# Kernel tuning notes

Measured on AMD Instinct MI355X. Metric: run time of the kernel, lower is better.

## Reference

```python
import jax, jax.numpy as jnp
import numpy as np

B, S, D, H = 2, 2048, 1024, 16
DH = D // H  # 64


def setup_inputs() -> dict:
    key = jax.random.key(0)
    ks = jax.random.split(key, 9)
    s = 1.0 / np.sqrt(D)
    return {
        "x": jax.random.normal(ks[0], (B, S, D), dtype=jnp.float32),
        "Wq": jax.random.normal(ks[1], (D, D), dtype=jnp.float32) * s,
        "bq": jnp.zeros((D,), dtype=jnp.float32),
        "Wk": jax.random.normal(ks[2], (D, D), dtype=jnp.float32) * s,
        "bk": jnp.zeros((D,), dtype=jnp.float32),
        "Wv": jax.random.normal(ks[3], (D, D), dtype=jnp.float32) * s,
        "bv": jnp.zeros((D,), dtype=jnp.float32),
        "Wo": jax.random.normal(ks[4], (D, D), dtype=jnp.float32) * s,
        "bo": jnp.zeros((D,), dtype=jnp.float32),
    }


def _split_heads(t):
    # [B, S, D] -> [B, H, S, DH]
    return t.reshape(B, S, H, DH).transpose(0, 2, 1, 3)


def reference(x, Wq, bq, Wk, bk, Wv, bv, Wo, bo):
    q = _split_heads(x @ Wq + bq)
    k = _split_heads(x @ Wk + bk)
    v = _split_heads(x @ Wv + bv)
    scale = 1.0 / jnp.sqrt(jnp.asarray(DH, dtype=x.dtype))
    # [B, H, S, S] score matrix (materialized, as in the original)
    logits = jnp.einsum("bhqd,bhkd->bhqk", q, k) * scale
    attn = jax.nn.softmax(logits, axis=-1)
    out = jnp.einsum("bhqk,bhkd->bhqd", attn, v)
    out = out.transpose(0, 2, 1, 3).reshape(B, S, D)
    return out @ Wo + bo
```

## Files before the change

### kernel.cpp

```cpp
#include <hip/hip_runtime.h>
#include <hip/hip_bf16.h>
#include <stdint.h>


typedef __attribute__((ext_vector_type(8))) short bf16x8;
typedef __attribute__((ext_vector_type(4))) float f32x4;

__device__ __forceinline__ void gld16(const void* g, void* l) {
  __builtin_amdgcn_global_load_lds((const __attribute__((address_space(1))) void*)g,
                                   (__attribute__((address_space(3))) void*)l, 16, 0, 0);
}

__device__ __forceinline__ unsigned short f2b(float f) {
  __hip_bfloat16 h = __float2bfloat16(f);
  return *reinterpret_cast<unsigned short*>(&h);
}

__global__ __launch_bounds__(256) void prep_kernel(const float* __restrict__ x,
                                                   const float* __restrict__ Wq,
                                                   const float* __restrict__ Wk,
                                                   const float* __restrict__ Wv,
                                                   const float* __restrict__ Wo,
                                                   unsigned short* __restrict__ xb,
                                                   unsigned short* __restrict__ wt) {
  __shared__ unsigned short Ls[64 * 72];
  int bid = blockIdx.x;
  int t = threadIdx.x;
  if (bid < 4096) {
    int i = (bid * 256 + t) * 4;
    float4 v = *(const float4*)(x + i);
    ushort4 o = make_ushort4(f2b(v.x), f2b(v.y), f2b(v.z), f2b(v.w));
    *(ushort4*)(xb + i) = o;
    return;
  }
  int tid = bid - 4096;
  int z = tid >> 8, rem = tid & 255;
  int bx = rem & 15, by = rem >> 4;
  const float* src = (z == 0) ? Wq : (z == 1) ? Wk : (z == 2) ? Wv : Wo;
  unsigned short* dst = wt + (size_t)z * 1024 * 1024;
  int k0 = bx * 64, n0 = by * 64;
  int c4 = t & 15;
#pragma unroll
  for (int it = 0; it < 4; ++it) {
    int row = it * 16 + (t >> 4);
    float4 v = *(const float4*)(src + (k0 + row) * 1024 + n0 + c4 * 4);
    Ls[(c4 * 4 + 0) * 72 + row] = f2b(v.x);
    Ls[(c4 * 4 + 1) * 72 + row] = f2b(v.y);
    Ls[(c4 * 4 + 2) * 72 + row] = f2b(v.z);
    Ls[(c4 * 4 + 3) * 72 + row] = f2b(v.w);
  }
  __syncthreads();
  int nr = t >> 2, kc = (t & 3) * 16;
  *(uint4*)(dst + (size_t)(n0 + nr) * 1024 + k0 + kc) = *(uint4*)&Ls[nr * 72 + kc];
  *(uint4*)(dst + (size_t)(n0 + nr) * 1024 + k0 + kc + 8) = *(uint4*)&Ls[nr * 72 + kc + 8];
}

__global__ __launch_bounds__(256) void gemm_qkv(const unsigned short* __restrict__ Ab,
                                                const unsigned short* __restrict__ Bt,
                                                const float* __restrict__ bq,
                                                const float* __restrict__ bk,
                                                const float* __restrict__ bv,
                                                unsigned short* __restrict__ qb,
                                                unsigned short* __restrict__ kb,
                                                unsigned short* __restrict__ vtb) {
  __shared__ unsigned short As[128 * 32];
  __shared__ unsigned short Bs[128 * 32];
  __shared__ unsigned short Es[128 * 72];
  const int t = threadIdx.x;
  const int lane = t & 63, wave = t >> 6;
  const int m0 = blockIdx.x * 128, n0 = blockIdx.y * 128;
  const int wr = (wave >> 1) * 64, wc = (wave & 1) * 64;
  const int fr = lane & 15, fq = lane >> 4;
  f32x4 acc[4][4] = {};
  for (int kt = 0; kt < 32; ++kt) {
    const unsigned short* Ag = Ab + (size_t)m0 * 1024 + kt * 32;
    const unsigned short* Bg = Bt + (size_t)n0 * 1024 + kt * 32;
#pragma unroll
    for (int rep = 0; rep < 2; ++rep) {
      int c = t + rep * 256;
      int row = c >> 2, col = (c & 3) * 8;
      gld16(Ag + (size_t)row * 1024 + col, (void*)(As + c * 8));
      gld16(Bg + (size_t)row * 1024 + col, (void*)(Bs + c * 8));
    }
    __syncthreads();
    bf16x8 a[4], b[4];
#pragma unroll
    for (int i = 0; i < 4; ++i) a[i] = *(const bf16x8*)&As[(wr + i * 16 + fr) * 32 + fq * 8];
#pragma unroll
    for (int j = 0; j < 4; ++j) b[j] = *(const bf16x8*)&Bs[(wc + j * 16 + fr) * 32 + fq * 8];
#pragma unroll
    for (int i = 0; i < 4; ++i)
#pragma unroll
      for (int j = 0; j < 4; ++j)
        acc[i][j] = __builtin_amdgcn_mfma_f32_16x16x32_bf16(a[i], b[j], acc[i][j], 0, 0, 0);
    __syncthreads();
  }
  const int which = n0 >> 10;
  const int bidx = m0 >> 11, s0 = m0 & 2047;
  if (which == 2) {
#pragma unroll
    for (int nh = 0; nh < 2; ++nh) {
      if ((wc >> 6) == nh) {
#pragma unroll
        for (int j = 0; j < 4; ++j) {
          int col = j * 16 + fr;
          float bias = bv[(n0 + nh * 64 + col) & 1023];
#pragma unroll
          for (int i = 0; i < 4; ++i) {
            int sl = wr + i * 16 + fq * 4;
            ushort4 pk;
            pk.x = f2b(acc[i][j][0] + bias);
            pk.y = f2b(acc[i][j][1] + bias);
            pk.z = f2b(acc[i][j][2] + bias);
            pk.w = f2b(acc[i][j][3] + bias);
            *(uint2*)&Es[col * 136 + sl] = *(uint2*)&pk;
          }
        }
      }
      __syncthreads();
      int h = ((n0 + nh * 64) & 1023) >> 6;
#pragma unroll
      for (int it = 0; it < 4; ++it) {
        int dh = it * 16 + (t >> 4);
        int ck = (t & 15) * 8;
        uint4 vv = *(uint4*)&Es[dh * 136 + ck];
        *(uint4*)&vtb[(size_t)((bidx * 16 + h) * 64 + dh) * 2048 + s0 + ck] = vv;
      }
      __syncthreads();
    }
  } else {
    unsigned short* dst = (which == 0) ? qb : kb;
    const float* bias_p = (which == 0) ? bq : bk;
    float scale = (which == 0) ? 0.1803368801111204f : 1.0f;
#pragma unroll
    for (int nh = 0; nh < 2; ++nh) {
      if ((wc >> 6) == nh) {
#pragma unroll
        for (int j = 0; j < 4; ++j) {
          int col = j * 16 + fr;
          float bias = bias_p[(n0 + nh * 64 + col) & 1023];
#pragma unroll
          for (int i = 0; i < 4; ++i)
#pragma unroll
            for (int r = 0; r < 4; ++r) {
              int sl = wr + i * 16 + fq * 4 + r;
              Es[sl * 72 + col] = f2b((acc[i][j][r] + bias) * scale);
            }
        }
      }
      __syncthreads();
      int h = ((n0 + nh * 64) & 1023) >> 6;
#pragma unroll
      for (int it = 0; it < 4; ++it) {
        int sl = it * 32 + (t >> 3);
        int ck = (t & 7) * 8;
        uint4 vv = *(uint4*)&Es[sl * 72 + ck];
        *(uint4*)&dst[(size_t)((bidx * 16 + h) * 2048 + s0 + sl) * 64 + ck] = vv;
      }
      __syncthreads();
    }
  }
}

__global__ __launch_bounds__(256, 2) void attn_kernel(const unsigned short* __restrict__ qb,
                                                      const unsigned short* __restrict__ kb,
                                                      const unsigned short* __restrict__ vtb,
                                                      unsigned short* __restrict__ attn) {
  __shared__ unsigned short Ks[2 * 4096];
  __shared__ unsigned short Vs[2 * 4096];
  __shared__ unsigned short Ps[4 * 2048];
  const int t = threadIdx.x, lane = t & 63, w = t >> 6;
  const int fr = lane & 15, fq = lane >> 4;
  const int bh = blockIdx.y, q0 = blockIdx.x * 128;
  const unsigned short* qg = qb + (size_t)bh * 2048 * 64;
  const unsigned short* kg0 = kb + (size_t)bh * 2048 * 64;
  const unsigned short* vg0 = vtb + (size_t)bh * 64 * 2048;

  bf16x8 qf[2][2];
#pragma unroll
  for (int nb = 0; nb < 2; ++nb)
#pragma unroll
    for (int kk = 0; kk < 2; ++kk)
      qf[nb][kk] = *(const bf16x8*)(qg + (size_t)(q0 + w * 32 + nb * 16 + fr) * 64 + kk * 32 + fq * 8);

  bf16x8 ones;
#pragma unroll
  for (int i = 0; i < 8; ++i) ones[i] = (short)0x3F80;

  f32x4 oacc[2][4] = {};
  f32x4 lacc[2] = {};
  unsigned short* Pw = Ps + w * 2048;

  {
#pragma unroll
    for (int rep = 0; rep < 2; ++rep) {
      int c = t + rep * 256;
      int kk = c >> 8, row = (c >> 2) & 63, cc = c & 3;
      gld16(kg0 + row * 64 + kk * 32 + cc * 8, (void*)(Ks + c * 8));
      gld16(vg0 + (size_t)row * 2048 + kk * 32 + cc * 8, (void*)(Vs + c * 8));
    }
  }

  for (int kt = 0; kt < 32; ++kt) {
    int buf = kt & 1;
    __syncthreads();
    if (kt + 1 < 32) {
      const unsigned short* kg = kg0 + (size_t)(kt + 1) * 4096;
      const unsigned short* vg = vg0 + (kt + 1) * 64;
      int lb = (buf ^ 1) * 4096;
#pragma unroll
      for (int rep = 0; rep < 2; ++rep) {
        int c = t + rep * 256;
        int kk = c >> 8, row = (c >> 2) & 63, cc = c & 3;
        gld16(kg + row * 64 + kk * 32 + cc * 8, (void*)(Ks + lb + c * 8));
        gld16(vg + (size_t)row * 2048 + kk * 32 + cc * 8, (void*)(Vs + lb + c * 8));
      }
    }
    const unsigned short* Kb = Ks + buf * 4096;
    const unsigned short* Vb = Vs + buf * 4096;
    f32x4 sacc[4][2] = {};
#pragma unroll
    for (int kk = 0; kk < 2; ++kk) {
      bf16x8 kf[4];
#pragma unroll
      for (int m = 0; m < 4; ++m) kf[m] = *(const bf16x8*)&Kb[kk * 2048 + (m * 16 + fr) * 32 + fq * 8];
#pragma unroll
      for (int m = 0; m < 4; ++m)
#pragma unroll
        for (int nb = 0; nb < 2; ++nb)
          sacc[m][nb] = __builtin_amdgcn_mfma_f32_16x16x32_bf16(kf[m], qf[nb][kk], sacc[m][nb], 0, 0, 0);
    }
#pragma unroll
    for (int m = 0; m < 4; ++m)
#pragma unroll
      for (int nb = 0; nb < 2; ++nb) {
        int qw = nb * 16 + fr;
        int G = (m * 2 + (fq >> 1)) ^ (qw & 7);
        ushort4 pk;
        pk.x = f2b(__builtin_amdgcn_exp2f(sacc[m][nb][0]));
        pk.y = f2b(__builtin_amdgcn_exp2f(sacc[m][nb][1]));
        pk.z = f2b(__builtin_amdgcn_exp2f(sacc[m][nb][2]));
        pk.w = f2b(__builtin_amdgcn_exp2f(sacc[m][nb][3]));
        *(uint2*)&Pw[qw * 64 + G * 8 + (fq & 1) * 4] = *(uint2*)&pk;
      }
#pragma unroll
    for (int kk = 0; kk < 2; ++kk) {
      bf16x8 pf[2];
#pragma unroll
      for (int mb = 0; mb < 2; ++mb) {
        int qw = mb * 16 + fr;
        int G = (kk * 4 + fq) ^ (qw & 7);
        pf[mb] = *(const bf16x8*)&Pw[qw * 64 + G * 8];
      }
#pragma unroll
      for (int n = 0; n < 4; ++n) {
        bf16x8 vf = *(const bf16x8*)&Vb[kk * 2048 + (n * 16 + fr) * 32 + fq * 8];
#pragma unroll
        for (int mb = 0; mb < 2; ++mb)
          oacc[mb][n] = __builtin_amdgcn_mfma_f32_16x16x32_bf16(pf[mb], vf, oacc[mb][n], 0, 0, 0);
      }
#pragma unroll
      for (int mb = 0; mb < 2; ++mb)
        lacc[mb] = __builtin_amdgcn_mfma_f32_16x16x32_bf16(pf[mb], ones, lacc[mb], 0, 0, 0);
    }
  }
  int bidx = bh >> 4, h = bh & 15;
#pragma unroll
  for (int mb = 0; mb < 2; ++mb)
#pragma unroll
    for (int r = 0; r < 4; ++r) {
      float inv = 1.f / lacc[mb][r];
      int s = q0 + w * 32 + mb * 16 + fq * 4 + r;
      size_t base = (size_t)(bidx * 2048 + s) * 1024 + h * 64;
#pragma unroll
      for (int n = 0; n < 4; ++n) attn[base + n * 16 + fr] = f2b(oacc[mb][n][r] * inv);
    }
}

__global__ __launch_bounds__(256) void gemm_out(const unsigned short* __restrict__ Ab,
                                                const unsigned short* __restrict__ Bt,
                                                const float* __restrict__ bo,
                                                float* __restrict__ out) {
  __shared__ unsigned short As[128 * 32];
  __shared__ unsigned short Bs[128 * 32];
  const int t = threadIdx.x;
  const int lane = t & 63, wave = t >> 6;
  const int m0 = blockIdx.x * 128, n0 = blockIdx.y * 128;
  const int wr = (wave >> 1) * 64, wc = (wave & 1) * 64;
  const int fr = lane & 15, fq = lane >> 4;
  f32x4 acc[4][4] = {};
  for (int kt = 0; kt < 32; ++kt) {
    const unsigned short* Ag = Ab + (size_t)m0 * 1024 + kt * 32;
    const unsigned short* Bg = Bt + (size_t)n0 * 1024 + kt * 32;
#pragma unroll
    for (int rep = 0; rep < 2; ++rep) {
      int c = t + rep * 256;
      int row = c >> 2, col = (c & 3) * 8;
      gld16(Ag + (size_t)row * 1024 + col, (void*)(As + c * 8));
      gld16(Bg + (size_t)row * 1024 + col, (void*)(Bs + c * 8));
    }
    __syncthreads();
    bf16x8 a[4], b[4];
#pragma unroll
    for (int i = 0; i < 4; ++i) a[i] = *(const bf16x8*)&As[(wr + i * 16 + fr) * 32 + fq * 8];
#pragma unroll
    for (int j = 0; j < 4; ++j) b[j] = *(const bf16x8*)&Bs[(wc + j * 16 + fr) * 32 + fq * 8];
#pragma unroll
    for (int i = 0; i < 4; ++i)
#pragma unroll
      for (int j = 0; j < 4; ++j)
        acc[i][j] = __builtin_amdgcn_mfma_f32_16x16x32_bf16(a[i], b[j], acc[i][j], 0, 0, 0);
    __syncthreads();
  }
#pragma unroll
  for (int j = 0; j < 4; ++j) {
    int gn = n0 + wc + j * 16 + fr;
    float bias = bo[gn];
#pragma unroll
    for (int i = 0; i < 4; ++i)
#pragma unroll
      for (int r = 0; r < 4; ++r) {
        int gm = m0 + wr + i * 16 + fq * 4 + r;
        out[(size_t)gm * 1024 + gn] = acc[i][j][r] + bias;
      }
  }
}

extern "C" void kernel_launch(void* const* d_in, const int* in_sizes, int n_in,
                              void* d_out, int out_size, void* d_ws, size_t ws_size,
                              hipStream_t stream) {
  const float* x = (const float*)d_in[0];
  const float* Wq = (const float*)d_in[1];
  const float* bq = (const float*)d_in[2];
  const float* Wk = (const float*)d_in[3];
  const float* bk = (const float*)d_in[4];
  const float* Wv = (const float*)d_in[5];
  const float* bv = (const float*)d_in[6];
  const float* Wo = (const float*)d_in[7];
  const float* bo = (const float*)d_in[8];
  float* out = (float*)d_out;

  unsigned short* ws = (unsigned short*)d_ws;
  const size_t MI = (size_t)1024 * 1024;
  unsigned short* xb = ws;
  unsigned short* wt = ws + 4 * MI;
  unsigned short* qb = wt + 4 * MI;
  unsigned short* kb = qb + 4 * MI;
  unsigned short* vtb = kb + 4 * MI;
  unsigned short* attn = xb;

  prep_kernel<<<5120, 256, 0, stream>>>(x, Wq, Wk, Wv, Wo, xb, wt);
  gemm_qkv<<<dim3(32, 24), 256, 0, stream>>>(xb, wt, bq, bk, bv, qb, kb, vtb);
  attn_kernel<<<dim3(16, 32), 256, 0, stream>>>(qb, kb, vtb, attn);
  gemm_out<<<dim3(32, 8), 256, 0, stream>>>(attn, wt + 3 * MI, bo, out);
}
```

Measured before the change: 209.3 us.

## Split attention keys across waves with 32x32 MFMA and register-resident P

Restructures the attention kernel so each wave handles all 128 queries but a disjoint 32-key slice of each key tile. Scores use 32x32x16 MFMAs, and probabilities stay in registers via a cross-half shuffle instead of round-tripping through LDS. Partial outputs and row sums are reduced across waves through shared memory at the end. Per-wave K/V loads use XOR swizzling and have no double buffering or block barrier in the main loop, so load latency is no longer hidden by prefetch and there is extra reduction work in the epilogue.

```diff
diff --git a/kernel.cpp b/kernel.cpp
--- a/kernel.cpp
+++ b/kernel.cpp
@@ -5,6 +5,7 @@
 
 typedef __attribute__((ext_vector_type(8))) short bf16x8;
 typedef __attribute__((ext_vector_type(4))) float f32x4;
+typedef __attribute__((ext_vector_type(16))) float f32x16;
 
 __device__ __forceinline__ void gld16(const void* g, void* l) {
   __builtin_amdgcn_global_load_lds((const __attribute__((address_space(1))) void*)g,
@@ -14,6 +15,10 @@
 __device__ __forceinline__ unsigned short f2b(float f) {
   __hip_bfloat16 h = __float2bfloat16(f);
   return *reinterpret_cast<unsigned short*>(&h);
+}
+
+__device__ __forceinline__ unsigned int pk2(float a, float b) {
+  return (unsigned int)f2b(a) | ((unsigned int)f2b(b) << 16);
 }
 
 __global__ __launch_bounds__(256) void prep_kernel(const float* __restrict__ x,
@@ -166,115 +171,127 @@
                                                       const unsigned short* __restrict__ kb,
                                                       const unsigned short* __restrict__ vtb,
                                                       unsigned short* __restrict__ attn) {
-  __shared__ unsigned short Ks[2 * 4096];
-  __shared__ unsigned short Vs[2 * 4096];
-  __shared__ unsigned short Ps[4 * 2048];
+  __shared__ unsigned short arena[16384];
+  __shared__ float Obuf[64 * 68];
+  __shared__ float Lbuf[128];
   const int t = threadIdx.x, lane = t & 63, w = t >> 6;
-  const int fr = lane & 15, fq = lane >> 4;
+  const int l31 = lane & 31, h = lane >> 5;
   const int bh = blockIdx.y, q0 = blockIdx.x * 128;
   const unsigned short* qg = qb + (size_t)bh * 2048 * 64;
   const unsigned short* kg0 = kb + (size_t)bh * 2048 * 64;
   const unsigned short* vg0 = vtb + (size_t)bh * 64 * 2048;
 
-  bf16x8 qf[2][2];
-#pragma unroll
-  for (int nb = 0; nb < 2; ++nb)
-#pragma unroll
-    for (int kk = 0; kk < 2; ++kk)
-      qf[nb][kk] = *(const bf16x8*)(qg + (size_t)(q0 + w * 32 + nb * 16 + fr) * 64 + kk * 32 + fq * 8);
-
-  bf16x8 ones;
-#pragma unroll
-  for (int i = 0; i < 8; ++i) ones[i] = (short)0x3F80;
-
-  f32x4 oacc[2][4] = {};
-  f32x4 lacc[2] = {};
-  unsigned short* Pw = Ps + w * 2048;
-
-  {
-#pragma unroll
-    for (int rep = 0; rep < 2; ++rep) {
-      int c = t + rep * 256;
-      int kk = c >> 8, row = (c >> 2) & 63, cc = c & 3;
-      gld16(kg0 + row * 64 + kk * 32 + cc * 8, (void*)(Ks + c * 8));
-      gld16(vg0 + (size_t)row * 2048 + kk * 32 + cc * 8, (void*)(Vs + c * 8));
-    }
-  }
-
-  for (int kt = 0; kt < 32; ++kt) {
-    int buf = kt & 1;
-    __syncthreads();
-    if (kt + 1 < 32) {
-      const unsigned short* kg = kg0 + (size_t)(kt + 1) * 4096;
-      const unsigned short* vg = vg0 + (kt + 1) * 64;
-      int lb = (buf ^ 1) * 4096;
-#pragma unroll
-      for (int rep = 0; rep < 2; ++rep) {
-        int c = t + rep * 256;
-        int kk = c >> 8, row = (c >> 2) & 63, cc = c & 3;
-        gld16(kg + row * 64 + kk * 32 + cc * 8, (void*)(Ks + lb + c * 8));
-        gld16(vg + (size_t)row * 2048 + kk * 32 + cc * 8, (void*)(Vs + lb + c * 8));
-      }
-    }
-    const unsigned short* Kb = Ks + buf * 4096;
-    const unsigned short* Vb = Vs + buf * 4096;
-    f32x4 sacc[4][2] = {};
-#pragma unroll
-    for (int kk = 0; kk < 2; ++kk) {
-      bf16x8 kf[4];
-#pragma unroll
-      for (int m = 0; m < 4; ++m) kf[m] = *(const bf16x8*)&Kb[kk * 2048 + (m * 16 + fr) * 32 + fq * 8];
-#pragma unroll
-      for (int m = 0; m < 4; ++m)
-#pragma unroll
-        for (int nb = 0; nb < 2; ++nb)
-          sacc[m][nb] = __builtin_amdgcn_mfma_f32_16x16x32_bf16(kf[m], qf[nb][kk], sacc[m][nb], 0, 0, 0);
-    }
-#pragma unroll
-    for (int m = 0; m < 4; ++m)
-#pragma unroll
-      for (int nb = 0; nb < 2; ++nb) {
-        int qw = nb * 16 + fr;
-        int G = (m * 2 + (fq >> 1)) ^ (qw & 7);
-        ushort4 pk;
-        pk.x = f2b(__builtin_amdgcn_exp2f(sacc[m][nb][0]));
-        pk.y = f2b(__builtin_amdgcn_exp2f(sacc[m][nb][1]));
-        pk.z = f2b(__builtin_amdgcn_exp2f(sacc[m][nb][2]));
-        pk.w = f2b(__builtin_amdgcn_exp2f(sacc[m][nb][3]));
-        *(uint2*)&Pw[qw * 64 + G * 8 + (fq & 1) * 4] = *(uint2*)&pk;
-      }
-#pragma unroll
-    for (int kk = 0; kk < 2; ++kk) {
-      bf16x8 pf[2];
-#pragma unroll
-      for (int mb = 0; mb < 2; ++mb) {
-        int qw = mb * 16 + fr;
-        int G = (kk * 4 + fq) ^ (qw & 7);
-        pf[mb] = *(const bf16x8*)&Pw[qw * 64 + G * 8];
-      }
-#pragma unroll
-      for (int n = 0; n < 4; ++n) {
-        bf16x8 vf = *(const bf16x8*)&Vb[kk * 2048 + (n * 16 + fr) * 32 + fq * 8];
-#pragma unroll
-        for (int mb = 0; mb < 2; ++mb)
-          oacc[mb][n] = __builtin_amdgcn_mfma_f32_16x16x32_bf16(pf[mb], vf, oacc[mb][n], 0, 0, 0);
-      }
-#pragma unroll
-      for (int mb = 0; mb < 2; ++mb)
-        lacc[mb] = __builtin_amdgcn_mfma_f32_16x16x32_bf16(pf[mb], ones, lacc[mb], 0, 0, 0);
-    }
-  }
-  int bidx = bh >> 4, h = bh & 15;
-#pragma unroll
-  for (int mb = 0; mb < 2; ++mb)
-#pragma unroll
-    for (int r = 0; r < 4; ++r) {
-      float inv = 1.f / lacc[mb][r];
-      int s = q0 + w * 32 + mb * 16 + fq * 4 + r;
-      size_t base = (size_t)(bidx * 2048 + s) * 1024 + h * 64;
-#pragma unroll
-      for (int n = 0; n < 4; ++n) attn[base + n * 16 + fr] = f2b(oacc[mb][n][r] * inv);
-    }
+  bf16x8 qf[4][4];
+#pragma unroll
+  for (int nb = 0; nb < 4; ++nb)
+#pragma unroll
+    for (int s = 0; s < 4; ++s)
+      qf[nb][s] = *(const bf16x8*)(qg + (size_t)(q0 + nb * 32 + l31) * 64 + s * 16 + h * 8);
+
+  unsigned short* Kw = arena + w * 4096;
+  unsigned short* Vw = Kw + 2048;
+  f32x16 oacc[4][2] = {};
+  float ladd[4] = {0.f, 0.f, 0.f, 0.f};
+
+  for (int kt = 0; kt < 16; ++kt) {
+    const int kbase = kt * 128 + w * 32;
+#pragma unroll
+    for (int i = 0; i < 4; ++i) {
+      int key = i * 8 + (lane >> 3), f = lane & 7, d = f ^ (key & 7);
+      gld16(kg0 + (size_t)(kbase + key) * 64 + d * 8, (void*)(Kw + (i * 64 + lane) * 8));
+    }
+#pragma unroll
+    for (int i = 0; i < 4; ++i) {
+      int dh = i * 16 + (lane >> 2), wf = lane & 3, ww = wf ^ (dh & 3);
+      gld16(vg0 + (size_t)dh * 2048 + kbase + ww * 8, (void*)(Vw + (i * 64 + lane) * 8));
+    }
+    bf16x8 kf[4];
+#pragma unroll
+    for (int s = 0; s < 4; ++s)
+      kf[s] = *(const bf16x8*)(Kw + (l31 * 8 + (((s * 2 + h) ^ (l31 & 7)))) * 8);
+    bf16x8 vf[2][2];
+#pragma unroll
+    for (int tt = 0; tt < 2; ++tt)
+#pragma unroll
+      for (int d2 = 0; d2 < 2; ++d2) {
+        int dh = d2 * 32 + l31;
+        vf[tt][d2] = *(const bf16x8*)(Vw + (dh * 4 + ((tt * 2 + h) ^ (dh & 3))) * 8);
+      }
+#pragma unroll
+    for (int nb = 0; nb < 4; ++nb) {
+      f32x16 sacc = {};
+#pragma unroll
+      for (int s = 0; s < 4; ++s)
+        sacc = __builtin_amdgcn_mfma_f32_32x32x16_bf16(kf[s], qf[nb][s], sacc, 0, 0, 0);
+      float p[16];
+      float rs = 0.f;
+#pragma unroll
+      for (int r = 0; r < 16; ++r) {
+        p[r] = __builtin_amdgcn_exp2f(sacc[r]);
+        rs += p[r];
+      }
+      ladd[nb] += rs;
+      unsigned int D[4][2];
+#pragma unroll
+      for (int g = 0; g < 4; ++g) {
+        D[g][0] = pk2(p[4 * g + 0], p[4 * g + 1]);
+        D[g][1] = pk2(p[4 * g + 2], p[4 * g + 3]);
+      }
+#pragma unroll
+      for (int tt = 0; tt < 2; ++tt) {
+        unsigned int Z0 = h ? D[2 * tt][0] : D[2 * tt + 1][0];
+        unsigned int Z1 = h ? D[2 * tt][1] : D[2 * tt + 1][1];
+        unsigned int X0 = (unsigned int)__shfl_xor((int)Z0, 32, 64);
+        unsigned int X1 = (unsigned int)__shfl_xor((int)Z1, 32, 64);
+        union { unsigned int u[4]; bf16x8 v; } uu;
+        uu.u[0] = h ? X0 : D[2 * tt][0];
+        uu.u[1] = h ? X1 : D[2 * tt][1];
+        uu.u[2] = h ? D[2 * tt + 1][0] : X0;
+        uu.u[3] = h ? D[2 * tt + 1][1] : X1;
+#pragma unroll
+        for (int d2 = 0; d2 < 2; ++d2)
+          oacc[nb][d2] = __builtin_amdgcn_mfma_f32_32x32x16_bf16(uu.v, vf[tt][d2], oacc[nb][d2], 0, 0, 0);
+      }
+    }
+  }
+#pragma unroll
+  for (int nb = 0; nb < 4; ++nb) ladd[nb] += __shfl_xor(ladd[nb], 32, 64);
+  __syncthreads();
+
+  const int bidx = bh >> 4, h16 = bh & 15;
+#pragma unroll
+  for (int p = 0; p < 2; ++p) {
+#pragma unroll
+    for (int k = 0; k < 4; ++k) {
+      int c = (w + k) & 3;
+      int nb = p * 2 + (c >> 1);
+#pragma unroll
+      for (int d2 = 0; d2 < 2; ++d2)
+#pragma unroll
+        for (int r2 = 0; r2 < 8; ++r2) {
+          int ql = c * 16 + (r2 & 3) + 8 * (r2 >> 2) + 4 * h;
+          int addr = ql * 68 + d2 * 32 + l31;
+          float v = oacc[nb][d2][(c & 1) * 8 + r2];
+          if (k == 0) Obuf[addr] = v; else Obuf[addr] += v;
+        }
+      if (p == 0 && h == 0) {
+        if (k == 0) Lbuf[c * 32 + l31] = ladd[c];
+        else Lbuf[c * 32 + l31] += ladd[c];
+      }
+      __syncthreads();
+    }
+    {
+      int row = t >> 2, q4 = t & 3, dh0 = q4 * 16;
+      float inv = 1.f / Lbuf[p * 64 + row];
+      unsigned short o[16];
+#pragma unroll
+      for (int i = 0; i < 16; ++i) o[i] = f2b(Obuf[row * 68 + dh0 + i] * inv);
+      size_t base = (size_t)(bidx * 2048 + q0 + p * 64 + row) * 1024 + h16 * 64 + dh0;
+      *(uint4*)&attn[base] = *(uint4*)&o[0];
+      *(uint4*)&attn[base + 8] = *(uint4*)&o[8];
+    }
+    __syncthreads();
+  }
 }
 
 __global__ __launch_bounds__(256) void gemm_out(const unsigned short* __restrict__ Ab,
```

New measurement: 292.1 us. 1.4x slower.
